# Kernel tuning notes

Hardware: AMD Instinct MI355X
Metric: run time of the kernel (lower is better)

The kernel has to match this reference:

```python
import jax, jax.numpy as jnp
import numpy as np

B, T, C, H, HS = 128, 256, 384, 6, 64

def setup_inputs() -> dict:
    key = jax.random.key(0)
    k1, k2, k3, k4, k5 = jax.random.split(key, 5)
    s = 0.02
    return {
        "x": jax.random.normal(k1, (B, T, C), dtype=jnp.float32),
        "Wq": jax.random.normal(k2, (H, C, HS), dtype=jnp.float32) * s,
        "Wk": jax.random.normal(k3, (H, C, HS), dtype=jnp.float32) * s,
        "Wv": jax.random.normal(k4, (H, C, HS), dtype=jnp.float32) * s,
        "Wp": jax.random.normal(k5, (C, C), dtype=jnp.float32) * s,
        "bp": jnp.zeros((C,), dtype=jnp.float32),
    }

def reference(x, Wq, Wk, Wv, Wp, bp):
    # per-head projections: [B,H,T,HS]
    q = jnp.einsum('btc,hcd->bhtd', x, Wq)
    k = jnp.einsum('btc,hcd->bhtd', x, Wk)
    v = jnp.einsum('btc,hcd->bhtd', x, Wv)
    scale = 1.0 / jnp.sqrt(jnp.asarray(HS, dtype=x.dtype))
    # scores: [B,H,T,T], causal mask then stable softmax
    scores = jnp.einsum('bhtd,bhsd->bhts', q, k) * scale
    causal = jnp.tril(jnp.ones((T, T), dtype=bool))
    scores = jnp.where(causal, scores, -jnp.inf)
    wei = jax.nn.softmax(scores, axis=-1)
    # dropout is identity in eval mode
    out = jnp.einsum('bhts,bhsd->bhtd', wei, v)  # [B,H,T,HS]
    out = out.transpose(0, 2, 1, 3).reshape(B, T, H * HS)  # concat heads
    return out @ Wp.T + bp  # output projection
```

## Files before the change

kernel.cpp:

```cpp
#include <hip/hip_runtime.h>
#include <hip/hip_bf16.h>
#include <math.h>

#define B_   128
#define T_   256
#define C_   384
#define H_   6
#define HS_  64
#define NTOK (B_*T_)
#define NQKV (3*C_)

typedef unsigned short u16;
typedef __attribute__((ext_vector_type(8))) short bf16x8;
typedef __attribute__((ext_vector_type(4))) float f32x4;

__device__ __forceinline__ u16 f2b(float f) {
    unsigned int u = __builtin_bit_cast(unsigned int, f);
    unsigned int r = (u + 0x7FFFu + ((u >> 16) & 1u)) >> 16;
    return (u16)r;
}

__device__ __forceinline__ float fexp2(float x) {
#if __has_builtin(__builtin_amdgcn_exp2f)
    return __builtin_amdgcn_exp2f(x);
#else
    return exp2f(x);
#endif
}

__device__ __forceinline__ void gl2lds16(const u16* g, u16* l) {
    __builtin_amdgcn_global_load_lds(
        (const __attribute__((address_space(1))) unsigned int*)g,
        (__attribute__((address_space(3))) unsigned int*)l, 16, 0, 0);
}

#define QSCALE 0.180336880f

#define J0_ (NTOK*C_/8)
#define J2_ (C_*C_/8)
#define J1_ (NQKV*C_)

__global__ __launch_bounds__(256) void prep(
    const float* __restrict__ x,  const float* __restrict__ Wq,
    const float* __restrict__ Wk, const float* __restrict__ Wv,
    const float* __restrict__ Wp,
    u16* __restrict__ xb, u16* __restrict__ wct, u16* __restrict__ wpb)
{
    int i = blockIdx.x * 256 + threadIdx.x;
    if (i < J0_) {
        const float4* s = (const float4*)x + (size_t)i * 2;
        float4 a = s[0], b = s[1];
        ushort4 o1, o2;
        o1.x = f2b(a.x); o1.y = f2b(a.y); o1.z = f2b(a.z); o1.w = f2b(a.w);
        o2.x = f2b(b.x); o2.y = f2b(b.y); o2.z = f2b(b.z); o2.w = f2b(b.w);
        ((ushort4*)xb)[(size_t)i * 2]     = o1;
        ((ushort4*)xb)[(size_t)i * 2 + 1] = o2;
    } else if (i < J0_ + J2_) {
        int j = i - J0_;
        const float4* s = (const float4*)Wp + (size_t)j * 2;
        float4 a = s[0], b = s[1];
        ushort4 o1, o2;
        o1.x = f2b(a.x); o1.y = f2b(a.y); o1.z = f2b(a.z); o1.w = f2b(a.w);
        o2.x = f2b(b.x); o2.y = f2b(b.y); o2.z = f2b(b.z); o2.w = f2b(b.w);
        ((ushort4*)wpb)[(size_t)j * 2]     = o1;
        ((ushort4*)wpb)[(size_t)j * 2 + 1] = o2;
    } else {
        int j = i - J0_ - J2_;
        if (j < J1_) {
            int n = j / C_, c = j % C_;
            int p = n / C_, rem = n % C_;
            int h = rem >> 6, d = rem & 63;
            const float* W = (p == 0 ? Wq : (p == 1 ? Wk : Wv));
            wct[j] = f2b(W[(h * C_ + c) * HS_ + d]);
        }
    }
}

__global__ __launch_bounds__(256) void gemm_qkv(
    const u16* __restrict__ xb, const u16* __restrict__ wct,
    u16* __restrict__ qo, u16* __restrict__ ko, u16* __restrict__ vt)
{
    __shared__ __align__(16) u16 As[128 * 64];
    __shared__ __align__(16) u16 Bs[128 * 64];

    const int gid  = blockIdx.x;
    const int xcd  = gid & 7;
    const int j_   = gid >> 3;
    const int colb = j_ % 9;
    const int rowb = (j_ / 9) * 8 + xcd;
    const int m0g  = rowb * 128;
    const int n0g  = colb * 128;

    const int tid = threadIdx.x;
    const int w = tid >> 6, lane = tid & 63;
    const int lm = lane & 15, qd = lane >> 4;
    const int wm = (w & 1) * 64, wn = (w >> 1) * 64;

    const int srow   = w * 32 + (lane >> 3);
    const int schunk = (lane & 7) ^ ((lane >> 3) & 7);
    const u16* gA = xb  + (size_t)(m0g + srow) * C_ + schunk * 8;
    const u16* gB = wct + (size_t)(n0g + srow) * C_ + schunk * 8;
    u16* lA = &As[(w * 32) * 64];
    u16* lB = &Bs[(w * 32) * 64];

    f32x4 acc[4][4];
    #pragma unroll
    for (int mi = 0; mi < 4; ++mi)
        #pragma unroll
        for (int ni = 0; ni < 4; ++ni)
            acc[mi][ni] = (f32x4){0.f, 0.f, 0.f, 0.f};

    for (int k0 = 0; k0 < C_; k0 += 64) {
        __syncthreads();
        #pragma unroll
        for (int j = 0; j < 4; ++j) {
            gl2lds16(gA + j * 8 * C_, lA + j * 8 * 64);
            gl2lds16(gB + j * 8 * C_, lB + j * 8 * 64);
        }
        gA += 64; gB += 64;
        __syncthreads();

        #pragma unroll
        for (int ks = 0; ks < 2; ++ks) {
            bf16x8 af[4], bfr[4];
            #pragma unroll
            for (int mi = 0; mi < 4; ++mi) {
                const int row = wm + mi * 16 + lm;
                const int sl = (ks * 4 + qd) ^ (lm & 7);
                af[mi] = *(const bf16x8*)&As[row * 64 + sl * 8];
            }
            #pragma unroll
            for (int ni = 0; ni < 4; ++ni) {
                const int row = wn + ni * 16 + lm;
                const int sl = (ks * 4 + qd) ^ (lm & 7);
                bfr[ni] = *(const bf16x8*)&Bs[row * 64 + sl * 8];
            }
            #pragma unroll
            for (int mi = 0; mi < 4; ++mi)
                #pragma unroll
                for (int ni = 0; ni < 4; ++ni)
                    acc[mi][ni] = __builtin_amdgcn_mfma_f32_16x16x32_bf16(
                        af[mi], bfr[ni], acc[mi][ni], 0, 0, 0);
        }
    }

    const int bI = m0g >> 8;
    const int tBase = m0g & 255;

    if (colb < 6) {
        u16* dst = (colb < 3) ? qo : ko;
        const float scl = (colb < 3) ? QSCALE : 1.0f;
        const int hBase = (colb % 3) * 2;
        u16 (*tb)[140] = (u16(*)[140])As;
        const int rloc = tid >> 3;
        const int mg   = rloc >> 4;
        #pragma unroll
        for (int mi = 0; mi < 4; ++mi) {
            __syncthreads();
            #pragma unroll
            for (int ni = 0; ni < 4; ++ni)
                #pragma unroll
                for (int r = 0; r < 4; ++r)
                    tb[(w & 1) * 16 + qd * 4 + r][wn + ni * 16 + lm]
                        = f2b(acc[mi][ni][r] * scl);
            __syncthreads();
            const int t = tBase + mg * 64 + mi * 16 + (rloc & 15);
            #pragma unroll
            for (int j = 0; j < 2; ++j) {
                const int col = (tid & 7) * 8 + j * 64;
                const int h = hBase + (col >> 6);
                bf16x8 vv = *(const bf16x8*)&tb[rloc][col];
                *(bf16x8*)(dst + ((size_t)(bI * H_ + h) * T_ + t) * HS_ + (col & 63)) = vv;
            }
        }
    } else {
        #pragma unroll
        for (int mi = 0; mi < 4; ++mi) {
            #pragma unroll
            for (int ni = 0; ni < 4; ++ni) {
                const int nn = (colb - 6) * 128 + wn + ni * 16 + lm;
                const int h = nn >> 6, d = nn & 63;
                const int t0 = tBase + wm + mi * 16 + qd * 4;
                ushort4 sv;
                sv.x = f2b(acc[mi][ni][0]); sv.y = f2b(acc[mi][ni][1]);
                sv.z = f2b(acc[mi][ni][2]); sv.w = f2b(acc[mi][ni][3]);
                *(ushort4*)(vt + ((size_t)(bI * H_ + h) * HS_ + d) * T_ + t0) = sv;
            }
        }
    }
}

__global__ __launch_bounds__(256) void attn_mfma(
    const u16* __restrict__ q, const u16* __restrict__ k,
    const u16* __restrict__ vt, u16* __restrict__ yb)
{
    __shared__ __align__(16) u16 Ks[256 * 64];
    __shared__ __align__(16) u16 Vs[64 * 256];
    __shared__ __align__(16) u16 Ps[4][16 * 72];

    const int bh = blockIdx.x;
    const int qt = blockIdx.y;
    const int b = bh / H_, h = bh % H_;
    const int tid = threadIdx.x, w = tid >> 6, lane = tid & 63;
    const int lm = lane & 15, qd = lane >> 4;

    const u16* qb = q  + (size_t)bh * T_ * HS_;
    const u16* kb = k  + (size_t)bh * T_ * HS_;
    const u16* vb = vt + (size_t)bh * HS_ * T_;

    const int t0 = qt * 128 + w * 16;

    bf16x8 aq[2][2];
    #pragma unroll
    for (int rg = 0; rg < 2; ++rg) {
        const u16* qrow = qb + (size_t)(t0 + rg * 64 + lm) * HS_;
        aq[rg][0] = *(const bf16x8*)(qrow + qd * 8);
        aq[rg][1] = *(const bf16x8*)(qrow + 32 + qd * 8);
    }

    #pragma unroll
    for (int j = 0; j < 8; ++j) {
        {
            const int L = (j * 4 + w) * 64 + lane;
            const int row = L >> 3;
            const int c = (L & 7) ^ (row & 7);
            gl2lds16(kb + (size_t)row * HS_ + c * 8, &Ks[(size_t)(j * 4 + w) * 512]);
        }
        {
            const int L = (j * 4 + w) * 64 + lane;
            const int d = L >> 5;
            const int c = (L & 31) ^ (d & 15);
            gl2lds16(vb + (size_t)d * T_ + c * 8, &Vs[(size_t)(j * 4 + w) * 512]);
        }
    }

    f32x4 acc[2][4];
    float ms[2][4], ls[2][4];
    #pragma unroll
    for (int rg = 0; rg < 2; ++rg) {
        #pragma unroll
        for (int ni = 0; ni < 4; ++ni) acc[rg][ni] = (f32x4){0.f, 0.f, 0.f, 0.f};
        #pragma unroll
        for (int r = 0; r < 4; ++r) { ms[rg][r] = -INFINITY; ls[rg][r] = 0.f; }
    }

    __syncthreads();

    u16* Pw = &Ps[w][0];
    const int nkt = (qt + 1) * 2;
    for (int kt = 0; kt < nkt; ++kt) {
        const int j0 = kt * 64;
        #pragma unroll
        for (int rg = 0; rg < 2; ++rg) {
            const int trg = t0 + rg * 64;
            if (j0 > trg + 15) continue;
            const bool needmask = (j0 + 63 > trg);

            f32x4 st[4];
            #pragma unroll
            for (int ni = 0; ni < 4; ++ni) st[ni] = (f32x4){0.f, 0.f, 0.f, 0.f};
            #pragma unroll
            for (int ks = 0; ks < 2; ++ks) {
                #pragma unroll
                for (int ni = 0; ni < 4; ++ni) {
                    const int row = j0 + ni * 16 + lm;
                    const int sl = (ks * 4 + qd) ^ (lm & 7);
                    bf16x8 bk = *(const bf16x8*)&Ks[row * 64 + sl * 8];
                    st[ni] = __builtin_amdgcn_mfma_f32_16x16x32_bf16(
                        aq[rg][ks], bk, st[ni], 0, 0, 0);
                }
            }

            float vals[4][4], rowmax[4];
            #pragma unroll
            for (int r = 0; r < 4; ++r) rowmax[r] = -INFINITY;
            #pragma unroll
            for (int ni = 0; ni < 4; ++ni) {
                const int s_g = j0 + ni * 16 + lm;
                #pragma unroll
                for (int r = 0; r < 4; ++r) {
                    float sc = st[ni][r];
                    if (needmask) {
                        const int t_g = trg + qd * 4 + r;
                        sc = (s_g > t_g) ? -1e30f : sc;
                    }
                    vals[ni][r] = sc;
                    rowmax[r] = fmaxf(rowmax[r], sc);
                }
            }
            #pragma unroll
            for (int msk = 1; msk <= 8; msk <<= 1)
                #pragma unroll
                for (int r = 0; r < 4; ++r)
                    rowmax[r] = fmaxf(rowmax[r], __shfl_xor(rowmax[r], msk, 64));

            float corr[4], rowsum[4];
            #pragma unroll
            for (int r = 0; r < 4; ++r) {
                const float mn = fmaxf(ms[rg][r], rowmax[r]);
                corr[r] = fexp2(ms[rg][r] - mn);
                ms[rg][r] = mn;
                rowsum[r] = 0.f;
            }
            #pragma unroll
            for (int ni = 0; ni < 4; ++ni) {
                #pragma unroll
                for (int r = 0; r < 4; ++r) {
                    const float p = fexp2(vals[ni][r] - ms[rg][r]);
                    rowsum[r] += p;
                    Pw[(qd * 4 + r) * 72 + ni * 16 + lm] = f2b(p);
                }
            }
            #pragma unroll
            for (int msk = 1; msk <= 8; msk <<= 1)
                #pragma unroll
                for (int r = 0; r < 4; ++r)
                    rowsum[r] += __shfl_xor(rowsum[r], msk, 64);
            #pragma unroll
            for (int r = 0; r < 4; ++r) ls[rg][r] = ls[rg][r] * corr[r] + rowsum[r];
            #pragma unroll
            for (int ni = 0; ni < 4; ++ni)
                #pragma unroll
                for (int r = 0; r < 4; ++r)
                    acc[rg][ni][r] *= corr[r];

            #pragma unroll
            for (int ks = 0; ks < 2; ++ks) {
                bf16x8 pa = *(const bf16x8*)&Pw[lm * 72 + ks * 32 + qd * 8];
                #pragma unroll
                for (int ni = 0; ni < 4; ++ni) {
                    const int d = ni * 16 + lm;
                    const int c = ((j0 >> 3) + ks * 4 + qd) ^ lm;
                    bf16x8 bv = *(const bf16x8*)&Vs[d * 256 + c * 8];
                    acc[rg][ni] = __builtin_amdgcn_mfma_f32_16x16x32_bf16(
                        pa, bv, acc[rg][ni], 0, 0, 0);
                }
            }
        }
    }

    __syncthreads();
    u16 (*yt)[72] = (u16(*)[72])Ks;
    #pragma unroll
    for (int rg = 0; rg < 2; ++rg)
        #pragma unroll
        for (int r = 0; r < 4; ++r) {
            const float inv = 1.f / ls[rg][r];
            #pragma unroll
            for (int ni = 0; ni < 4; ++ni)
                yt[w * 16 + rg * 64 + qd * 4 + r][ni * 16 + lm]
                    = f2b(acc[rg][ni][r] * inv);
        }
    __syncthreads();
    #pragma unroll
    for (int rr = 0; rr < 4; ++rr) {
        const int row = rr * 32 + (tid >> 3);
        const int col = (tid & 7) * 8;
        bf16x8 vv = *(const bf16x8*)&yt[row][col];
        const int t_g = qt * 128 + row;
        *(bf16x8*)(yb + ((size_t)(b * T_ + t_g)) * C_ + h * 64 + col) = vv;
    }
}

__global__ __launch_bounds__(256) void gemm_proj(
    const u16* __restrict__ yb, const u16* __restrict__ wpb,
    const float* __restrict__ bp, float* __restrict__ out)
{
    __shared__ __align__(16) u16 SMEM[128 * 64 * 2];
    u16* As = SMEM;
    u16* Bs = SMEM + 128 * 64;

    const int gid  = blockIdx.x;
    const int xcd  = gid & 7;
    const int j_   = gid >> 3;
    const int colb = j_ % 3;
    const int rowb = (j_ / 3) * 8 + xcd;
    const int m0g  = rowb * 128;
    const int n0g  = colb * 128;

    const int tid = threadIdx.x;
    const int w = tid >> 6, lane = tid & 63;
    const int lm = lane & 15, qd = lane >> 4;
    const int wm = (w & 1) * 64, wn = (w >> 1) * 64;

    const int srow   = w * 32 + (lane >> 3);
    const int schunk = (lane & 7) ^ ((lane >> 3) & 7);
    const u16* gA = yb  + (size_t)(m0g + srow) * C_ + schunk * 8;
    const u16* gB = wpb + (size_t)(n0g + srow) * C_ + schunk * 8;
    u16* lA = &As[(w * 32) * 64];
    u16* lB = &Bs[(w * 32) * 64];

    f32x4 acc[4][4];
    #pragma unroll
    for (int mi = 0; mi < 4; ++mi)
        #pragma unroll
        for (int ni = 0; ni < 4; ++ni)
            acc[mi][ni] = (f32x4){0.f, 0.f, 0.f, 0.f};

    for (int k0 = 0; k0 < C_; k0 += 64) {
        __syncthreads();
        #pragma unroll
        for (int j = 0; j < 4; ++j) {
            gl2lds16(gA + j * 8 * C_, lA + j * 8 * 64);
            gl2lds16(gB + j * 8 * C_, lB + j * 8 * 64);
        }
        gA += 64; gB += 64;
        __syncthreads();

        #pragma unroll
        for (int ks = 0; ks < 2; ++ks) {
            bf16x8 af[4], bfr[4];
            #pragma unroll
            for (int mi = 0; mi < 4; ++mi) {
                const int row = wm + mi * 16 + lm;
                const int sl = (ks * 4 + qd) ^ (lm & 7);
                af[mi] = *(const bf16x8*)&As[row * 64 + sl * 8];
            }
            #pragma unroll
            for (int ni = 0; ni < 4; ++ni) {
                const int row = wn + ni * 16 + lm;
                const int sl = (ks * 4 + qd) ^ (lm & 7);
                bfr[ni] = *(const bf16x8*)&Bs[row * 64 + sl * 8];
            }
            #pragma unroll
            for (int mi = 0; mi < 4; ++mi)
                #pragma unroll
                for (int ni = 0; ni < 4; ++ni)
                    acc[mi][ni] = __builtin_amdgcn_mfma_f32_16x16x32_bf16(
                        af[mi], bfr[ni], acc[mi][ni], 0, 0, 0);
        }
    }

    float bpv[4];
    #pragma unroll
    for (int ni = 0; ni < 4; ++ni) bpv[ni] = bp[n0g + wn + ni * 16 + lm];

    float (*tb)[134] = (float(*)[134])SMEM;
    const int rloc = tid >> 3;
    const int mg   = rloc >> 4;
    #pragma unroll
    for (int mi = 0; mi < 4; ++mi) {
        __syncthreads();
        #pragma unroll
        for (int ni = 0; ni < 4; ++ni)
            #pragma unroll
            for (int r = 0; r < 4; ++r)
                tb[(w & 1) * 16 + qd * 4 + r][wn + ni * 16 + lm]
                    = acc[mi][ni][r] + bpv[ni];
        __syncthreads();
        const int m = m0g + mg * 64 + mi * 16 + (rloc & 15);
        #pragma unroll
        for (int j = 0; j < 4; ++j) {
            const int col = (tid & 7) * 4 + j * 32;
            float4 vv = *(const float4*)&tb[rloc][col];
            *(float4*)(out + (size_t)m * C_ + n0g + col) = vv;
        }
    }
}

extern "C" void kernel_launch(void* const* d_in, const int* in_sizes, int n_in,
                              void* d_out, int out_size, void* d_ws, size_t ws_size,
                              hipStream_t stream)
{
    const float* x  = (const float*)d_in[0];
    const float* Wq = (const float*)d_in[1];
    const float* Wk = (const float*)d_in[2];
    const float* Wv = (const float*)d_in[3];
    const float* Wp = (const float*)d_in[4];
    const float* bp = (const float*)d_in[5];
    float* out = (float*)d_out;

    u16* xb  = (u16*)d_ws;
    u16* wct = xb  + (size_t)NTOK * C_;
    u16* wpb = wct + (size_t)NQKV * C_;
    u16* qo  = wpb + (size_t)C_ * C_;
    u16* ko  = qo  + (size_t)B_ * H_ * T_ * HS_;
    u16* vt  = ko  + (size_t)B_ * H_ * T_ * HS_;
    u16* yb  = vt  + (size_t)B_ * H_ * T_ * HS_;

    const int prep_blocks = (J0_ + J2_ + J1_ + 255) / 256;
    hipLaunchKernelGGL(prep, dim3(prep_blocks), dim3(256), 0, stream,
                       x, Wq, Wk, Wv, Wp, xb, wct, wpb);

    hipLaunchKernelGGL(gemm_qkv, dim3(NTOK / 128 * (NQKV / 128)), dim3(256), 0, stream,
                       xb, wct, qo, ko, vt);

    hipLaunchKernelGGL(attn_mfma, dim3(B_ * H_, T_ / 128), dim3(256), 0, stream,
                       qo, ko, vt, yb);

    hipLaunchKernelGGL(gemm_proj, dim3(NTOK / 128 * (C_ / 128)), dim3(256), 0, stream,
                       yb, wpb, bp, out);
}
```

Baseline: 220.3 us.

## Use 256-row GEMM tiles with 512 threads and stream K/V in attention

Both projection GEMMs now use 512-thread blocks over 256x128 output tiles, so each loaded weight tile serves twice as many rows and half as many blocks are launched. The attention kernel no longer stages the full 256-key K and V^T in shared memory. It loads them in 128-key phases, only as many as the causal mask needs, which cuts shared memory per block so more blocks can be resident (launch bound of 3). The costs are an extra barrier per phase and larger GEMM blocks, which may reduce how well blocks fill the compute units.

After: 196.4 us. 1.12x faster.

```diff
diff --git a/kernel.cpp b/kernel.cpp
--- a/kernel.cpp
+++ b/kernel.cpp
@@ -76,11 +76,11 @@
     }
 }
 
-__global__ __launch_bounds__(256) void gemm_qkv(
+__global__ __launch_bounds__(512, 4) void gemm_qkv(
     const u16* __restrict__ xb, const u16* __restrict__ wct,
     u16* __restrict__ qo, u16* __restrict__ ko, u16* __restrict__ vt)
 {
-    __shared__ __align__(16) u16 As[128 * 64];
+    __shared__ __align__(16) u16 As[256 * 64];
     __shared__ __align__(16) u16 Bs[128 * 64];
 
     const int gid  = blockIdx.x;
@@ -88,20 +88,19 @@
     const int j_   = gid >> 3;
     const int colb = j_ % 9;
     const int rowb = (j_ / 9) * 8 + xcd;
-    const int m0g  = rowb * 128;
+    const int m0g  = rowb * 256;
     const int n0g  = colb * 128;
 
     const int tid = threadIdx.x;
     const int w = tid >> 6, lane = tid & 63;
     const int lm = lane & 15, qd = lane >> 4;
-    const int wm = (w & 1) * 64, wn = (w >> 1) * 64;
-
-    const int srow   = w * 32 + (lane >> 3);
+    const int wm = (w >> 1) * 64, wn = (w & 1) * 64;
+
     const int schunk = (lane & 7) ^ ((lane >> 3) & 7);
-    const u16* gA = xb  + (size_t)(m0g + srow) * C_ + schunk * 8;
-    const u16* gB = wct + (size_t)(n0g + srow) * C_ + schunk * 8;
+    const u16* gA = xb  + (size_t)(m0g + w * 32 + (lane >> 3)) * C_ + schunk * 8;
+    const u16* gB = wct + (size_t)(n0g + w * 16 + (lane >> 3)) * C_ + schunk * 8;
     u16* lA = &As[(w * 32) * 64];
-    u16* lB = &Bs[(w * 32) * 64];
+    u16* lB = &Bs[(w * 16) * 64];
 
     f32x4 acc[4][4];
     #pragma unroll
@@ -113,10 +112,11 @@
     for (int k0 = 0; k0 < C_; k0 += 64) {
         __syncthreads();
         #pragma unroll
-        for (int j = 0; j < 4; ++j) {
+        for (int j = 0; j < 4; ++j)
             gl2lds16(gA + j * 8 * C_, lA + j * 8 * 64);
+        #pragma unroll
+        for (int j = 0; j < 2; ++j)
             gl2lds16(gB + j * 8 * C_, lB + j * 8 * 64);
-        }
         gA += 64; gB += 64;
         __syncthreads();
 
@@ -145,15 +145,13 @@
     }
 
     const int bI = m0g >> 8;
-    const int tBase = m0g & 255;
 
     if (colb < 6) {
         u16* dst = (colb < 3) ? qo : ko;
         const float scl = (colb < 3) ? QSCALE : 1.0f;
         const int hBase = (colb % 3) * 2;
-        u16 (*tb)[140] = (u16(*)[140])As;
+        u16 (*tb)[136] = (u16(*)[136])As;
         const int rloc = tid >> 3;
-        const int mg   = rloc >> 4;
         #pragma unroll
         for (int mi = 0; mi < 4; ++mi) {
             __syncthreads();
@@ -161,16 +159,16 @@
             for (int ni = 0; ni < 4; ++ni)
                 #pragma unroll
                 for (int r = 0; r < 4; ++r)
-                    tb[(w & 1) * 16 + qd * 4 + r][wn + ni * 16 + lm]
+                    tb[(w >> 1) * 16 + qd * 4 + r][wn + ni * 16 + lm]
                         = f2b(acc[mi][ni][r] * scl);
             __syncthreads();
-            const int t = tBase + mg * 64 + mi * 16 + (rloc & 15);
-            #pragma unroll
-            for (int j = 0; j < 2; ++j) {
-                const int col = (tid & 7) * 8 + j * 64;
-                const int h = hBase + (col >> 6);
-                bf16x8 vv = *(const bf16x8*)&tb[rloc][col];
-                *(bf16x8*)(dst + ((size_t)(bI * H_ + h) * T_ + t) * HS_ + (col & 63)) = vv;
+            const int t = (rloc >> 4) * 64 + mi * 16 + (rloc & 15);
+            #pragma unroll
+            for (int jj = 0; jj < 2; ++jj) {
+                const int cc = (tid & 7) * 8 + jj * 64;
+                const int h = hBase + (cc >> 6);
+                bf16x8 vv = *(const bf16x8*)&tb[rloc][cc];
+                *(bf16x8*)(dst + ((size_t)(bI * H_ + h) * T_ + t) * HS_ + (cc & 63)) = vv;
             }
         }
     } else {
@@ -180,7 +178,7 @@
             for (int ni = 0; ni < 4; ++ni) {
                 const int nn = (colb - 6) * 128 + wn + ni * 16 + lm;
                 const int h = nn >> 6, d = nn & 63;
-                const int t0 = tBase + wm + mi * 16 + qd * 4;
+                const int t0 = wm + mi * 16 + qd * 4;
                 ushort4 sv;
                 sv.x = f2b(acc[mi][ni][0]); sv.y = f2b(acc[mi][ni][1]);
                 sv.z = f2b(acc[mi][ni][2]); sv.w = f2b(acc[mi][ni][3]);
@@ -190,13 +188,14 @@
     }
 }
 
-__global__ __launch_bounds__(256) void attn_mfma(
+__global__ __launch_bounds__(256, 3) void attn_mfma(
     const u16* __restrict__ q, const u16* __restrict__ k,
     const u16* __restrict__ vt, u16* __restrict__ yb)
 {
-    __shared__ __align__(16) u16 Ks[256 * 64];
-    __shared__ __align__(16) u16 Vs[64 * 256];
-    __shared__ __align__(16) u16 Ps[4][16 * 72];
+    __shared__ __align__(16) u16 SM[128 * 64 + 64 * 128 + 4 * 16 * 72];
+    u16* Ks = SM;
+    u16* Vs = SM + 8192;
+    u16* Ps = SM + 16384;
 
     const int bh = blockIdx.x;
     const int qt = blockIdx.y;
@@ -218,22 +217,6 @@
         aq[rg][1] = *(const bf16x8*)(qrow + 32 + qd * 8);
     }
 
-    #pragma unroll
-    for (int j = 0; j < 8; ++j) {
-        {
-            const int L = (j * 4 + w) * 64 + lane;
-            const int row = L >> 3;
-            const int c = (L & 7) ^ (row & 7);
-            gl2lds16(kb + (size_t)row * HS_ + c * 8, &Ks[(size_t)(j * 4 + w) * 512]);
-        }
-        {
-            const int L = (j * 4 + w) * 64 + lane;
-            const int d = L >> 5;
-            const int c = (L & 31) ^ (d & 15);
-            gl2lds16(vb + (size_t)d * T_ + c * 8, &Vs[(size_t)(j * 4 + w) * 512]);
-        }
-    }
-
     f32x4 acc[2][4];
     float ms[2][4], ls[2][4];
     #pragma unroll
@@ -244,103 +227,121 @@
         for (int r = 0; r < 4; ++r) { ms[rg][r] = -INFINITY; ls[rg][r] = 0.f; }
     }
 
+    u16* Pw = &Ps[w * 16 * 72];
+    const int nph = qt + 1;
+
+    for (int p = 0; p < nph; ++p) {
+        if (p) __syncthreads();
+        #pragma unroll
+        for (int j = 0; j < 4; ++j) {
+            const int row = w * 32 + j * 8 + (lane >> 3);
+            const int c = (lane & 7) ^ (row & 7);
+            gl2lds16(kb + (size_t)(p * 128 + row) * HS_ + c * 8,
+                     &Ks[(w * 32 + j * 8) * 64]);
+        }
+        #pragma unroll
+        for (int j = 0; j < 4; ++j) {
+            const int d = w * 16 + j * 4 + (lane >> 4);
+            const int c = (lane & 15) ^ (d & 15);
+            gl2lds16(vb + (size_t)d * T_ + p * 128 + c * 8,
+                     &Vs[(w * 16 + j * 4) * 128]);
+        }
+        __syncthreads();
+
+        for (int kt2 = 0; kt2 < 2; ++kt2) {
+            const int j0 = p * 128 + kt2 * 64;
+            #pragma unroll
+            for (int rg = 0; rg < 2; ++rg) {
+                const int trg = t0 + rg * 64;
+                if (j0 > trg + 15) continue;
+                const bool needmask = (j0 + 63 > trg);
+
+                f32x4 st[4];
+                #pragma unroll
+                for (int ni = 0; ni < 4; ++ni) st[ni] = (f32x4){0.f, 0.f, 0.f, 0.f};
+                #pragma unroll
+                for (int ks = 0; ks < 2; ++ks) {
+                    #pragma unroll
+                    for (int ni = 0; ni < 4; ++ni) {
+                        const int lrow = kt2 * 64 + ni * 16 + lm;
+                        const int sl = (ks * 4 + qd) ^ (lm & 7);
+                        bf16x8 bk = *(const bf16x8*)&Ks[lrow * 64 + sl * 8];
+                        st[ni] = __builtin_amdgcn_mfma_f32_16x16x32_bf16(
+                            aq[rg][ks], bk, st[ni], 0, 0, 0);
+                    }
+                }
+
+                float vals[4][4], rowmax[4];
+                #pragma unroll
+                for (int r = 0; r < 4; ++r) rowmax[r] = -INFINITY;
+                #pragma unroll
+                for (int ni = 0; ni < 4; ++ni) {
+                    const int s_g = j0 + ni * 16 + lm;
+                    #pragma unroll
+                    for (int r = 0; r < 4; ++r) {
+                        float sc = st[ni][r];
+                        if (needmask) {
+                            const int t_g = trg + qd * 4 + r;
+                            sc = (s_g > t_g) ? -1e30f : sc;
+                        }
+                        vals[ni][r] = sc;
+                        rowmax[r] = fmaxf(rowmax[r], sc);
+                    }
+                }
+                #pragma unroll
+                for (int msk = 1; msk <= 8; msk <<= 1)
+                    #pragma unroll
+                    for (int r = 0; r < 4; ++r)
+                        rowmax[r] = fmaxf(rowmax[r], __shfl_xor(rowmax[r], msk, 64));
+
+                float corr[4], rowsum[4];
+                #pragma unroll
+                for (int r = 0; r < 4; ++r) {
+                    const float mn = fmaxf(ms[rg][r], rowmax[r]);
+                    corr[r] = fexp2(ms[rg][r] - mn);
+                    ms[rg][r] = mn;
+                    rowsum[r] = 0.f;
+                }
+                #pragma unroll
+                for (int ni = 0; ni < 4; ++ni) {
+                    #pragma unroll
+                    for (int r = 0; r < 4; ++r) {
+                        const float pv = fexp2(vals[ni][r] - ms[rg][r]);
+                        rowsum[r] += pv;
+                        Pw[(qd * 4 + r) * 72 + ni * 16 + lm] = f2b(pv);
+                    }
+                }
+                #pragma unroll
+                for (int msk = 1; msk <= 8; msk <<= 1)
+                    #pragma unroll
+                    for (int r = 0; r < 4; ++r)
+                        rowsum[r] += __shfl_xor(rowsum[r], msk, 64);
+                #pragma unroll
+                for (int r = 0; r < 4; ++r) ls[rg][r] = ls[rg][r] * corr[r] + rowsum[r];
+                #pragma unroll
+                for (int ni = 0; ni < 4; ++ni)
+                    #pragma unroll
+                    for (int r = 0; r < 4; ++r)
+                        acc[rg][ni][r] *= corr[r];
+
+                #pragma unroll
+                for (int ks = 0; ks < 2; ++ks) {
+                    bf16x8 pa = *(const bf16x8*)&Pw[lm * 72 + ks * 32 + qd * 8];
+                    #pragma unroll
+                    for (int ni = 0; ni < 4; ++ni) {
+                        const int d = ni * 16 + lm;
+                        const int c = (kt2 * 8 + ks * 4 + qd) ^ lm;
+                        bf16x8 bv = *(const bf16x8*)&Vs[d * 128 + c * 8];
+                        acc[rg][ni] = __builtin_amdgcn_mfma_f32_16x16x32_bf16(
+                            pa, bv, acc[rg][ni], 0, 0, 0);
+                    }
+                }
+            }
+        }
+    }
+
     __syncthreads();
-
-    u16* Pw = &Ps[w][0];
-    const int nkt = (qt + 1) * 2;
-    for (int kt = 0; kt < nkt; ++kt) {
-        const int j0 = kt * 64;
-        #pragma unroll
-        for (int rg = 0; rg < 2; ++rg) {
-            const int trg = t0 + rg * 64;
-            if (j0 > trg + 15) continue;
-            const bool needmask = (j0 + 63 > trg);
-
-            f32x4 st[4];
-            #pragma unroll
-            for (int ni = 0; ni < 4; ++ni) st[ni] = (f32x4){0.f, 0.f, 0.f, 0.f};
-            #pragma unroll
-            for (int ks = 0; ks < 2; ++ks) {
-                #pragma unroll
-                for (int ni = 0; ni < 4; ++ni) {
-                    const int row = j0 + ni * 16 + lm;
-                    const int sl = (ks * 4 + qd) ^ (lm & 7);
-                    bf16x8 bk = *(const bf16x8*)&Ks[row * 64 + sl * 8];
-                    st[ni] = __builtin_amdgcn_mfma_f32_16x16x32_bf16(
-                        aq[rg][ks], bk, st[ni], 0, 0, 0);
-                }
-            }
-
-            float vals[4][4], rowmax[4];
-            #pragma unroll
-            for (int r = 0; r < 4; ++r) rowmax[r] = -INFINITY;
-            #pragma unroll
-            for (int ni = 0; ni < 4; ++ni) {
-                const int s_g = j0 + ni * 16 + lm;
-                #pragma unroll
-                for (int r = 0; r < 4; ++r) {
-                    float sc = st[ni][r];
-                    if (needmask) {
-                        const int t_g = trg + qd * 4 + r;
-                        sc = (s_g > t_g) ? -1e30f : sc;
-                    }
-                    vals[ni][r] = sc;
-                    rowmax[r] = fmaxf(rowmax[r], sc);
-                }
-            }
-            #pragma unroll
-            for (int msk = 1; msk <= 8; msk <<= 1)
-                #pragma unroll
-                for (int r = 0; r < 4; ++r)
-                    rowmax[r] = fmaxf(rowmax[r], __shfl_xor(rowmax[r], msk, 64));
-
-            float corr[4], rowsum[4];
-            #pragma unroll
-            for (int r = 0; r < 4; ++r) {
-                const float mn = fmaxf(ms[rg][r], rowmax[r]);
-                corr[r] = fexp2(ms[rg][r] - mn);
-                ms[rg][r] = mn;
-                rowsum[r] = 0.f;
-            }
-            #pragma unroll
-            for (int ni = 0; ni < 4; ++ni) {
-                #pragma unroll
-                for (int r = 0; r < 4; ++r) {
-                    const float p = fexp2(vals[ni][r] - ms[rg][r]);
-                    rowsum[r] += p;
-                    Pw[(qd * 4 + r) * 72 + ni * 16 + lm] = f2b(p);
-                }
-            }
-            #pragma unroll
-            for (int msk = 1; msk <= 8; msk <<= 1)
-                #pragma unroll
-                for (int r = 0; r < 4; ++r)
-                    rowsum[r] += __shfl_xor(rowsum[r], msk, 64);
-            #pragma unroll
-            for (int r = 0; r < 4; ++r) ls[rg][r] = ls[rg][r] * corr[r] + rowsum[r];
-            #pragma unroll
-            for (int ni = 0; ni < 4; ++ni)
-                #pragma unroll
-                for (int r = 0; r < 4; ++r)
-                    acc[rg][ni][r] *= corr[r];
-
-            #pragma unroll
-            for (int ks = 0; ks < 2; ++ks) {
-                bf16x8 pa = *(const bf16x8*)&Pw[lm * 72 + ks * 32 + qd * 8];
-                #pragma unroll
-                for (int ni = 0; ni < 4; ++ni) {
-                    const int d = ni * 16 + lm;
-                    const int c = ((j0 >> 3) + ks * 4 + qd) ^ lm;
-                    bf16x8 bv = *(const bf16x8*)&Vs[d * 256 + c * 8];
-                    acc[rg][ni] = __builtin_amdgcn_mfma_f32_16x16x32_bf16(
-                        pa, bv, acc[rg][ni], 0, 0, 0);
-                }
-            }
-        }
-    }
-
-    __syncthreads();
-    u16 (*yt)[72] = (u16(*)[72])Ks;
+    u16 (*yt)[72] = (u16(*)[72])SM;
     #pragma unroll
     for (int rg = 0; rg < 2; ++rg)
         #pragma unroll
@@ -362,33 +363,32 @@
     }
 }
 
-__global__ __launch_bounds__(256) void gemm_proj(
+__global__ __launch_bounds__(512, 4) void gemm_proj(
     const u16* __restrict__ yb, const u16* __restrict__ wpb,
     const float* __restrict__ bp, float* __restrict__ out)
 {
-    __shared__ __align__(16) u16 SMEM[128 * 64 * 2];
+    __shared__ __align__(16) u16 SMEM[256 * 64 + 128 * 64];
     u16* As = SMEM;
-    u16* Bs = SMEM + 128 * 64;
+    u16* Bs = SMEM + 256 * 64;
 
     const int gid  = blockIdx.x;
     const int xcd  = gid & 7;
     const int j_   = gid >> 3;
     const int colb = j_ % 3;
     const int rowb = (j_ / 3) * 8 + xcd;
-    const int m0g  = rowb * 128;
+    const int m0g  = rowb * 256;
     const int n0g  = colb * 128;
 
     const int tid = threadIdx.x;
     const int w = tid >> 6, lane = tid & 63;
     const int lm = lane & 15, qd = lane >> 4;
-    const int wm = (w & 1) * 64, wn = (w >> 1) * 64;
-
-    const int srow   = w * 32 + (lane >> 3);
+    const int wm = (w >> 1) * 64, wn = (w & 1) * 64;
+
     const int schunk = (lane & 7) ^ ((lane >> 3) & 7);
-    const u16* gA = yb  + (size_t)(m0g + srow) * C_ + schunk * 8;
-    const u16* gB = wpb + (size_t)(n0g + srow) * C_ + schunk * 8;
+    const u16* gA = yb  + (size_t)(m0g + w * 32 + (lane >> 3)) * C_ + schunk * 8;
+    const u16* gB = wpb + (size_t)(n0g + w * 16 + (lane >> 3)) * C_ + schunk * 8;
     u16* lA = &As[(w * 32) * 64];
-    u16* lB = &Bs[(w * 32) * 64];
+    u16* lB = &Bs[(w * 16) * 64];
 
     f32x4 acc[4][4];
     #pragma unroll
@@ -400,10 +400,11 @@
     for (int k0 = 0; k0 < C_; k0 += 64) {
         __syncthreads();
         #pragma unroll
-        for (int j = 0; j < 4; ++j) {
+        for (int j = 0; j < 4; ++j)
             gl2lds16(gA + j * 8 * C_, lA + j * 8 * 64);
+        #pragma unroll
+        for (int j = 0; j < 2; ++j)
             gl2lds16(gB + j * 8 * C_, lB + j * 8 * 64);
-        }
         gA += 64; gB += 64;
         __syncthreads();
 
@@ -435,9 +436,8 @@
     #pragma unroll
     for (int ni = 0; ni < 4; ++ni) bpv[ni] = bp[n0g + wn + ni * 16 + lm];
 
-    float (*tb)[134] = (float(*)[134])SMEM;
+    float (*tb)[132] = (float(*)[132])SMEM;
     const int rloc = tid >> 3;
-    const int mg   = rloc >> 4;
     #pragma unroll
     for (int mi = 0; mi < 4; ++mi) {
         __syncthreads();
@@ -445,15 +445,15 @@
         for (int ni = 0; ni < 4; ++ni)
             #pragma unroll
             for (int r = 0; r < 4; ++r)
-                tb[(w & 1) * 16 + qd * 4 + r][wn + ni * 16 + lm]
+                tb[(w >> 1) * 16 + qd * 4 + r][wn + ni * 16 + lm]
                     = acc[mi][ni][r] + bpv[ni];
         __syncthreads();
-        const int m = m0g + mg * 64 + mi * 16 + (rloc & 15);
-        #pragma unroll
-        for (int j = 0; j < 4; ++j) {
-            const int col = (tid & 7) * 4 + j * 32;
-            float4 vv = *(const float4*)&tb[rloc][col];
-            *(float4*)(out + (size_t)m * C_ + n0g + col) = vv;
+        const int m = m0g + (rloc >> 4) * 64 + mi * 16 + (rloc & 15);
+        #pragma unroll
+        for (int jj = 0; jj < 4; ++jj) {
+            const int cc = (tid & 7) * 4 + jj * 32;
+            float4 vv = *(const float4*)&tb[rloc][cc];
+            *(float4*)(out + (size_t)m * C_ + n0g + cc) = vv;
         }
     }
 }
@@ -482,12 +482,12 @@
     hipLaunchKernelGGL(prep, dim3(prep_blocks), dim3(256), 0, stream,
                        x, Wq, Wk, Wv, Wp, xb, wct, wpb);
 
-    hipLaunchKernelGGL(gemm_qkv, dim3(NTOK / 128 * (NQKV / 128)), dim3(256), 0, stream,
+    hipLaunchKernelGGL(gemm_qkv, dim3((NTOK / 256) * (NQKV / 128)), dim3(512), 0, stream,
                        xb, wct, qo, ko, vt);
 
     hipLaunchKernelGGL(attn_mfma, dim3(B_ * H_, T_ / 128), dim3(256), 0, stream,
                        qo, ko, vt, yb);
 
-    hipLaunchKernelGGL(gemm_proj, dim3(NTOK / 128 * (C_ / 128)), dim3(256), 0, stream,
+    hipLaunchKernelGGL(gemm_proj, dim3((NTOK / 256) * (C_ / 128)), dim3(512), 0, stream,
                        yb, wpb, bp, out);
 }
```
